# Kernel tuning notes

Hardware: AMD Instinct MI355X
Metric: run time of the kernel (lower is better)

Reference implementation:

```python
import jax, jax.numpy as jnp
import numpy as np

BATCH, IN, HID, OUT = 8192, 1024, 4096, 1000

def _l2norm_rows(w):
    # matches F.normalize(p=2, dim=1) with eps=1e-12
    n = jnp.linalg.norm(w, axis=1, keepdims=True)
    return w / jnp.maximum(n, 1e-12)

def setup_inputs() -> dict:
    key = jax.random.key(0)
    k1, k2, k3 = jax.random.split(key, 3)
    x = jax.random.normal(k1, (BATCH, IN), dtype=jnp.float32)
    kohonen_w = _l2norm_rows(jax.random.normal(k2, (HID, IN), dtype=jnp.float32))
    grossberg_w = _l2norm_rows(jax.random.normal(k3, (OUT, HID), dtype=jnp.float32))
    return {"x": x, "kohonen_w": kohonen_w, "grossberg_w": grossberg_w}

def reference(x, kohonen_w, grossberg_w):
    # x: [B, D]; kohonen_w: [H, D]; grossberg_w: [O, H]
    x2 = jnp.sum(x * x, axis=1, keepdims=True)            # [B, 1]
    w2 = jnp.sum(kohonen_w * kohonen_w, axis=1)           # [H]
    d2 = x2 - 2.0 * (x @ kohonen_w.T) + w2[None, :]       # [B, H]
    winners = jnp.argmin(d2, axis=1)                      # [B] (argmin of dist == argmin of dist^2)
    # one-hot @ grossberg_w.T is exactly a row gather of grossberg_w.T
    output = grossberg_w.T[winners]                       # [B, O]
    return output, winners, x.shape[0]
```

## Files before the change

### kernel.cpp

```cpp
#include <hip/hip_runtime.h>
#include <stdint.h>

#define B_SZ 8192
#define D_SZ 1024
#define H_SZ 4096
#define O_SZ 1000

#define MARGIN 0.0625f

typedef float f32x4 __attribute__((ext_vector_type(4)));
typedef __bf16 bf16x8 __attribute__((ext_vector_type(8)));

static __device__ __forceinline__ uint16_t f2bf(float f) {
  uint32_t u = __float_as_uint(f);
  uint32_t r = (u + 0x7fffu + ((u >> 16) & 1u)) >> 16;
  return (uint16_t)r;
}

__global__ __launch_bounds__(256) void convert_bf16(const float* __restrict__ src,
                                                    ushort4* __restrict__ dst, int n4) {
  int i = blockIdx.x * blockDim.x + threadIdx.x;
  if (i < n4) {
    f32x4 v = reinterpret_cast<const f32x4*>(src)[i];
    ushort4 o;
    o.x = f2bf(v[0]); o.y = f2bf(v[1]); o.z = f2bf(v[2]); o.w = f2bf(v[3]);
    dst[i] = o;
  }
}

__global__ __launch_bounds__(64) void w2_kernel(const float* __restrict__ w,
                                                double* __restrict__ w2d) {
  const int h = blockIdx.x;
  const int l = threadIdx.x;
  const f32x4* wr = reinterpret_cast<const f32x4*>(w + (size_t)h * D_SZ);
  double s = 0.0;
#pragma unroll
  for (int j = 0; j < 4; ++j) {
    f32x4 v = wr[j * 64 + l];
    s += (double)v[0] * v[0] + (double)v[1] * v[1] + (double)v[2] * v[2] + (double)v[3] * v[3];
  }
#pragma unroll
  for (int m = 32; m; m >>= 1) s += __shfl_xor(s, m);
  if (l == 0) w2d[h] = s;
}

#define LPITCH 72
__global__ __launch_bounds__(256) void kohonen_gemm(const uint16_t* __restrict__ xb,
                                                    const uint16_t* __restrict__ wb,
                                                    float* __restrict__ tmax64,
                                                    unsigned long long* __restrict__ tmask64) {
  __shared__ uint16_t As[128 * LPITCH];
  __shared__ uint16_t Bs[128 * LPITCH];
  const int tid = threadIdx.x;
  const int bm = blockIdx.x, bn = blockIdx.y;
  const int lane = tid & 63, wv = tid >> 6;
  const int wm = wv >> 1, wn = wv & 1;
  f32x4 acc[4][4] = {};

  const int sr = tid >> 3;
  const int sp = tid & 7;
  const uint16_t* xrow = xb + (size_t)(bm * 128) * D_SZ;
  const uint16_t* wrow = wb + (size_t)(bn * 128) * D_SZ;

  for (int kt = 0; kt < D_SZ / 64; ++kt) {
    __syncthreads();
#pragma unroll
    for (int i = 0; i < 4; ++i) {
      const int r = sr + i * 32;
      const int4 va = *reinterpret_cast<const int4*>(xrow + (size_t)r * D_SZ + kt * 64 + sp * 8);
      *reinterpret_cast<int4*>(&As[r * LPITCH + sp * 8]) = va;
      const int4 vb = *reinterpret_cast<const int4*>(wrow + (size_t)r * D_SZ + kt * 64 + sp * 8);
      *reinterpret_cast<int4*>(&Bs[r * LPITCH + sp * 8]) = vb;
    }
    __syncthreads();
#pragma unroll
    for (int s = 0; s < 2; ++s) {
      bf16x8 a[4], b[4];
      const int col = s * 32 + (lane >> 4) * 8;
#pragma unroll
      for (int f = 0; f < 4; ++f) {
        a[f] = *reinterpret_cast<const bf16x8*>(&As[(wm * 64 + f * 16 + (lane & 15)) * LPITCH + col]);
        b[f] = *reinterpret_cast<const bf16x8*>(&Bs[(wn * 64 + f * 16 + (lane & 15)) * LPITCH + col]);
      }
#pragma unroll
      for (int fm = 0; fm < 4; ++fm)
#pragma unroll
        for (int fn = 0; fn < 4; ++fn)
          acc[fm][fn] = __builtin_amdgcn_mfma_f32_16x16x32_bf16(a[fm], b[fn], acc[fm][fn], 0, 0, 0);
    }
  }

  const int tile = bn * 2 + wn;
  const int colid = lane & 15;
  const int g = lane >> 4;
#pragma unroll
  for (int fm = 0; fm < 4; ++fm) {
    float v[4];
#pragma unroll
    for (int j = 0; j < 4; ++j)
      v[j] = fmaxf(fmaxf(acc[fm][0][j], acc[fm][1][j]), fmaxf(acc[fm][2][j], acc[fm][3][j]));
#pragma unroll
    for (int m = 1; m < 16; m <<= 1) {
#pragma unroll
      for (int j = 0; j < 4; ++j) v[j] = fmaxf(v[j], __shfl_xor(v[j], m));
    }
    unsigned long long mk[4];
#pragma unroll
    for (int j = 0; j < 4; ++j) {
      unsigned long long b = 0;
      const float thr = v[j] - MARGIN;
#pragma unroll
      for (int fn = 0; fn < 4; ++fn)
        if (acc[fm][fn][j] >= thr) b |= 1ull << (fn * 16 + colid);
      mk[j] = b;
    }
#pragma unroll
    for (int m = 1; m < 16; m <<= 1) {
#pragma unroll
      for (int j = 0; j < 4; ++j) mk[j] |= __shfl_xor(mk[j], m);
    }
    if (colid == 0) {
#pragma unroll
      for (int j = 0; j < 4; ++j) {
        const int row = bm * 128 + wm * 64 + fm * 16 + g * 4 + j;
        tmax64[(size_t)row * 64 + tile] = v[j];
        tmask64[(size_t)row * 64 + tile] = mk[j];
      }
    }
  }
}

__global__ __launch_bounds__(64) void rescore2(const float* __restrict__ x,
                                               const float* __restrict__ w,
                                               const double* __restrict__ w2d,
                                               const float* __restrict__ tmax64,
                                               const unsigned long long* __restrict__ tmask64,
                                               int* __restrict__ winners,
                                               float* __restrict__ winners_f) {
  const int row = blockIdx.x;
  const int l = threadIdx.x;

  f32x4 xr[4];
  const f32x4* xp = reinterpret_cast<const f32x4*>(x + (size_t)row * D_SZ);
#pragma unroll
  for (int j = 0; j < 4; ++j) xr[j] = xp[j * 64 + l];

  const float pmax = tmax64[(size_t)row * 64 + l];
  const unsigned long long pmask = tmask64[(size_t)row * 64 + l];
  float M = pmax;
#pragma unroll
  for (int m = 1; m < 64; m <<= 1) M = fmaxf(M, __shfl_xor(M, m));
  const float thr = M - MARGIN;

  double bestS = -1e300;
  int bestI = 0x7fffffff;

  unsigned long long bits = __ballot(pmax >= thr && pmask != 0ull);
  while (bits) {
    const int src = __ffsll(bits) - 1;
    unsigned long long tmask = __shfl(pmask, src);
    const int tile = src;
    while (tmask) {
      const int b = __ffsll(tmask) - 1;
      const int h = tile * 64 + b;
      const f32x4* wp = reinterpret_cast<const f32x4*>(w + (size_t)h * D_SZ);
      double dot = 0.0;
#pragma unroll
      for (int j = 0; j < 4; ++j) {
        f32x4 wv = wp[j * 64 + l];
        dot += (double)xr[j][0] * wv[0] + (double)xr[j][1] * wv[1] +
               (double)xr[j][2] * wv[2] + (double)xr[j][3] * wv[3];
      }
#pragma unroll
      for (int m = 32; m; m >>= 1) dot += __shfl_xor(dot, m);
      const double sc = 2.0 * dot - w2d[h];
      if (sc > bestS || (sc == bestS && h < bestI)) { bestS = sc; bestI = h; }
      tmask &= tmask - 1;
    }
    bits &= bits - 1;
  }

  if (l == 0) { winners[row] = bestI; winners_f[row] = (float)bestI; }
}

__global__ __launch_bounds__(256) void transpose_g(const float* __restrict__ g,
                                                   float* __restrict__ gt) {
  __shared__ float t[32][33];
  const int h0 = blockIdx.x * 32;
  const int o0 = blockIdx.y * 32;
  const int lx = threadIdx.x & 31, ly = threadIdx.x >> 5;
  for (int i = ly; i < 32; i += 8) {
    const int o = o0 + i;
    t[i][lx] = (o < O_SZ) ? g[(size_t)o * H_SZ + (h0 + lx)] : 0.f;
  }
  __syncthreads();
  for (int i = ly; i < 32; i += 8) {
    const int o = o0 + lx;
    if (o < O_SZ) gt[(size_t)(h0 + i) * O_SZ + o] = t[lx][i];
  }
}

__global__ __launch_bounds__(256) void gather_out(const float* __restrict__ gt,
                                                  const int* __restrict__ winners,
                                                  float* __restrict__ out) {
  const int row = blockIdx.x;
  const int wsel = winners[row];
  const f32x4* src = reinterpret_cast<const f32x4*>(gt + (size_t)wsel * O_SZ);
  f32x4* dst = reinterpret_cast<f32x4*>(out + (size_t)row * O_SZ);
  if (threadIdx.x < O_SZ / 4) dst[threadIdx.x] = src[threadIdx.x];
  if (row == 0 && threadIdx.x == 0)
    out[(size_t)B_SZ * O_SZ + B_SZ] = (float)B_SZ;
}

extern "C" void kernel_launch(void* const* d_in, const int* in_sizes, int n_in,
                              void* d_out, int out_size, void* d_ws, size_t ws_size,
                              hipStream_t stream) {
  const float* x  = (const float*)d_in[0];
  const float* kw = (const float*)d_in[1];
  const float* gw = (const float*)d_in[2];
  float* out = (float*)d_out;
  char* ws = (char*)d_ws;

  uint16_t*           xb   = (uint16_t*)(ws);
  uint16_t*           wb   = (uint16_t*)(ws + 16777216);
  float*              tmx  = (float*)   (ws + 25165824);
  unsigned long long* tmk  = (unsigned long long*)(ws + 27262976);
  int*                wins = (int*)     (ws + 31457280);
  double*             w2d  = (double*)  (ws + 31490048);
  float*              gt   = (float*)   (ws);

  convert_bf16<<<(B_SZ * D_SZ / 4 + 255) / 256, 256, 0, stream>>>(x, (ushort4*)xb, B_SZ * D_SZ / 4);
  convert_bf16<<<(H_SZ * D_SZ / 4 + 255) / 256, 256, 0, stream>>>(kw, (ushort4*)wb, H_SZ * D_SZ / 4);
  w2_kernel<<<H_SZ, 64, 0, stream>>>(kw, w2d);

  dim3 g1(B_SZ / 128, H_SZ / 128);
  kohonen_gemm<<<g1, 256, 0, stream>>>(xb, wb, tmx, tmk);

  rescore2<<<B_SZ, 64, 0, stream>>>(x, kw, w2d, tmx, tmk, wins, out + (size_t)B_SZ * O_SZ);

  dim3 g3(H_SZ / 32, (O_SZ + 31) / 32);
  transpose_g<<<g3, 256, 0, stream>>>(gw, gt);

  gather_out<<<B_SZ, 256, 0, stream>>>(gt, wins, out);
}
```

Measured before the change: 139.1 us.

## Load GEMM tiles directly into LDS with global_load_lds and XOR swizzle

Replaces the register-staged global-to-LDS copy in the Kohonen GEMM with direct global_load_lds DMA transfers of 16 bytes per lane. The padded LDS layout becomes an unpadded 128-byte-pitch layout, with an XOR swizzle applied on both the load mapping and the fragment reads to limit bank conflicts. This is meant to cut VGPR traffic and the instructions spent staging tiles, at the cost of an explicit vmcnt wait and a more fragile address mapping.

```diff
diff --git a/kernel.cpp b/kernel.cpp
--- a/kernel.cpp
+++ b/kernel.cpp
@@ -44,43 +44,60 @@
   if (l == 0) w2d[h] = s;
 }
 
-#define LPITCH 72
 __global__ __launch_bounds__(256) void kohonen_gemm(const uint16_t* __restrict__ xb,
                                                     const uint16_t* __restrict__ wb,
                                                     float* __restrict__ tmax64,
                                                     unsigned long long* __restrict__ tmask64) {
-  __shared__ uint16_t As[128 * LPITCH];
-  __shared__ uint16_t Bs[128 * LPITCH];
+  __shared__ uint16_t As[8192];
+  __shared__ uint16_t Bs[8192];
   const int tid = threadIdx.x;
   const int bm = blockIdx.x, bn = blockIdx.y;
   const int lane = tid & 63, wv = tid >> 6;
   const int wm = wv >> 1, wn = wv & 1;
   f32x4 acc[4][4] = {};
 
-  const int sr = tid >> 3;
-  const int sp = tid & 7;
   const uint16_t* xrow = xb + (size_t)(bm * 128) * D_SZ;
   const uint16_t* wrow = wb + (size_t)(bn * 128) * D_SZ;
 
+  int srow[4], spart[4];
+#pragma unroll
+  for (int i = 0; i < 4; ++i) {
+    const int c_lin = (wv * 4 + i) * 64 + lane;
+    const int c_src = c_lin ^ ((((c_lin >> 5) & 1)) << 1);
+    srow[i] = c_src >> 3;
+    spart[i] = c_src & 7;
+  }
+
+  const int r15 = lane & 15, g = lane >> 4;
+  const int xorv = (r15 & 4) ? 32 : 0;
+
   for (int kt = 0; kt < D_SZ / 64; ++kt) {
     __syncthreads();
 #pragma unroll
     for (int i = 0; i < 4; ++i) {
-      const int r = sr + i * 32;
-      const int4 va = *reinterpret_cast<const int4*>(xrow + (size_t)r * D_SZ + kt * 64 + sp * 8);
-      *reinterpret_cast<int4*>(&As[r * LPITCH + sp * 8]) = va;
-      const int4 vb = *reinterpret_cast<const int4*>(wrow + (size_t)r * D_SZ + kt * 64 + sp * 8);
-      *reinterpret_cast<int4*>(&Bs[r * LPITCH + sp * 8]) = vb;
-    }
+      const uint16_t* ga = xrow + (size_t)srow[i] * D_SZ + kt * 64 + spart[i] * 8;
+      __builtin_amdgcn_global_load_lds(
+          (const __attribute__((address_space(1))) uint32_t*)ga,
+          (__attribute__((address_space(3))) uint32_t*)((char*)As + ((wv * 4 + i) << 10)),
+          16, 0, 0);
+      const uint16_t* gb = wrow + (size_t)srow[i] * D_SZ + kt * 64 + spart[i] * 8;
+      __builtin_amdgcn_global_load_lds(
+          (const __attribute__((address_space(1))) uint32_t*)gb,
+          (__attribute__((address_space(3))) uint32_t*)((char*)Bs + ((wv * 4 + i) << 10)),
+          16, 0, 0);
+    }
+    asm volatile("s_waitcnt vmcnt(0)" ::: "memory");
     __syncthreads();
 #pragma unroll
     for (int s = 0; s < 2; ++s) {
       bf16x8 a[4], b[4];
-      const int col = s * 32 + (lane >> 4) * 8;
+      const int cb = s * 64 + g * 16;
 #pragma unroll
       for (int f = 0; f < 4; ++f) {
-        a[f] = *reinterpret_cast<const bf16x8*>(&As[(wm * 64 + f * 16 + (lane & 15)) * LPITCH + col]);
-        b[f] = *reinterpret_cast<const bf16x8*>(&Bs[(wn * 64 + f * 16 + (lane & 15)) * LPITCH + col]);
+        const int ra = (wm * 64 + f * 16 + r15) * 128 + cb;
+        a[f] = *reinterpret_cast<const bf16x8*>((const char*)As + (ra ^ xorv));
+        const int rb = (wn * 64 + f * 16 + r15) * 128 + cb;
+        b[f] = *reinterpret_cast<const bf16x8*>((const char*)Bs + (rb ^ xorv));
       }
 #pragma unroll
       for (int fm = 0; fm < 4; ++fm)
@@ -92,7 +109,6 @@
 
   const int tile = bn * 2 + wn;
   const int colid = lane & 15;
-  const int g = lane >> 4;
 #pragma unroll
   for (int fm = 0; fm < 4; ++fm) {
     float v[4];
@@ -107,12 +123,12 @@
     unsigned long long mk[4];
 #pragma unroll
     for (int j = 0; j < 4; ++j) {
-      unsigned long long b = 0;
+      unsigned long long bmask = 0;
       const float thr = v[j] - MARGIN;
 #pragma unroll
       for (int fn = 0; fn < 4; ++fn)
-        if (acc[fm][fn][j] >= thr) b |= 1ull << (fn * 16 + colid);
-      mk[j] = b;
+        if (acc[fm][fn][j] >= thr) bmask |= 1ull << (fn * 16 + colid);
+      mk[j] = bmask;
     }
 #pragma unroll
     for (int m = 1; m < 16; m <<= 1) {
```

After: 146.2 us. 5.1% more time.

## Rework Kohonen GEMM with async LDS double buffering and 32x32 MFMA

Applied to the files above, without the earlier changes.

Rewrites the bf16 GEMM main loop to stage tiles straight from global memory into LDS with global_load_lds, double-buffered so the next K tile loads while the current one computes. Uses XOR-swizzled LDS addressing instead of padding, and switches to 32x32x16 MFMA with four accumulators per wave. Also remaps block IDs to group tiles for cache locality and sets launch bounds for two blocks per CU. The epilogue is rewritten for the new accumulator layout. This adds hand-written waitcnt and barrier logic that must stay correct.

```diff
diff --git a/kernel.cpp b/kernel.cpp
--- a/kernel.cpp
+++ b/kernel.cpp
@@ -9,6 +9,7 @@
 #define MARGIN 0.0625f
 
 typedef float f32x4 __attribute__((ext_vector_type(4)));
+typedef float f32x16 __attribute__((ext_vector_type(16)));
 typedef __bf16 bf16x8 __attribute__((ext_vector_type(8)));
 
 static __device__ __forceinline__ uint16_t f2bf(float f) {
@@ -44,87 +45,98 @@
   if (l == 0) w2d[h] = s;
 }
 
-#define LPITCH 72
-__global__ __launch_bounds__(256) void kohonen_gemm(const uint16_t* __restrict__ xb,
-                                                    const uint16_t* __restrict__ wb,
-                                                    float* __restrict__ tmax64,
-                                                    unsigned long long* __restrict__ tmask64) {
-  __shared__ uint16_t As[128 * LPITCH];
-  __shared__ uint16_t Bs[128 * LPITCH];
+__global__ __launch_bounds__(256, 2) void kohonen_gemm(const uint16_t* __restrict__ xb,
+                                                       const uint16_t* __restrict__ wb,
+                                                       float* __restrict__ tmax64,
+                                                       unsigned long long* __restrict__ tmask64) {
+  __shared__ __align__(16) char As[32768];
+  __shared__ __align__(16) char Bs[32768];
   const int tid = threadIdx.x;
-  const int bm = blockIdx.x, bn = blockIdx.y;
   const int lane = tid & 63, wv = tid >> 6;
   const int wm = wv >> 1, wn = wv & 1;
-  f32x4 acc[4][4] = {};
-
-  const int sr = tid >> 3;
-  const int sp = tid & 7;
+  const int l31 = lane & 31, hi = lane >> 5;
+
+  const int bid = blockIdx.x;
+  const int wg = (bid & 7) * 256 + (bid >> 3);
+  const int bm = wg >> 5, bn = wg & 31;
+
   const uint16_t* xrow = xb + (size_t)(bm * 128) * D_SZ;
   const uint16_t* wrow = wb + (size_t)(bn * 128) * D_SZ;
 
-  for (int kt = 0; kt < D_SZ / 64; ++kt) {
-    __syncthreads();
+  f32x16 acc00 = {}, acc01 = {}, acc10 = {}, acc11 = {};
+
+  const int st_row = (lane >> 3);
+  const int st_part = (lane & 7) ^ (((lane >> 3) & 3) << 1);
+  auto stage = [&](int sp, int kt) {
 #pragma unroll
     for (int i = 0; i < 4; ++i) {
-      const int r = sr + i * 32;
-      const int4 va = *reinterpret_cast<const int4*>(xrow + (size_t)r * D_SZ + kt * 64 + sp * 8);
-      *reinterpret_cast<int4*>(&As[r * LPITCH + sp * 8]) = va;
-      const int4 vb = *reinterpret_cast<const int4*>(wrow + (size_t)r * D_SZ + kt * 64 + sp * 8);
-      *reinterpret_cast<int4*>(&Bs[r * LPITCH + sp * 8]) = vb;
-    }
-    __syncthreads();
-#pragma unroll
-    for (int s = 0; s < 2; ++s) {
-      bf16x8 a[4], b[4];
-      const int col = s * 32 + (lane >> 4) * 8;
-#pragma unroll
-      for (int f = 0; f < 4; ++f) {
-        a[f] = *reinterpret_cast<const bf16x8*>(&As[(wm * 64 + f * 16 + (lane & 15)) * LPITCH + col]);
-        b[f] = *reinterpret_cast<const bf16x8*>(&Bs[(wn * 64 + f * 16 + (lane & 15)) * LPITCH + col]);
-      }
-#pragma unroll
-      for (int fm = 0; fm < 4; ++fm)
-#pragma unroll
-        for (int fn = 0; fn < 4; ++fn)
-          acc[fm][fn] = __builtin_amdgcn_mfma_f32_16x16x32_bf16(a[fm], b[fn], acc[fm][fn], 0, 0, 0);
-    }
+      const int blk = wv * 4 + i;
+      const int row = blk * 8 + st_row;
+      const uint16_t* sa = xrow + (size_t)row * D_SZ + kt * 64 + st_part * 8;
+      __builtin_amdgcn_global_load_lds(
+          (const __attribute__((address_space(1))) uint32_t*)sa,
+          (__attribute__((address_space(3))) uint32_t*)(As + sp * 16384 + blk * 1024),
+          16, 0, 0);
+      const uint16_t* sb = wrow + (size_t)row * D_SZ + kt * 64 + st_part * 8;
+      __builtin_amdgcn_global_load_lds(
+          (const __attribute__((address_space(1))) uint32_t*)sb,
+          (__attribute__((address_space(3))) uint32_t*)(Bs + sp * 16384 + blk * 1024),
+          16, 0, 0);
+    }
+  };
+
+  auto ldfrag = [&](const char* base, int row, int ks) -> bf16x8 {
+    const int byte = (row * 128 + ks * 32 + hi * 16) ^ ((row & 3) << 5);
+    return *reinterpret_cast<const bf16x8*>(base + byte);
+  };
+
+  stage(0, 0);
+
+  for (int t = 0; t < 16; ++t) {
+    const int rp = t & 1, sp = rp ^ 1;
+    if (t < 15) {
+      stage(sp, t + 1);
+      asm volatile("s_waitcnt vmcnt(8)" ::: "memory");
+    } else {
+      asm volatile("s_waitcnt vmcnt(0)" ::: "memory");
+    }
+    __builtin_amdgcn_s_barrier();
+    const char* Ab = As + rp * 16384;
+    const char* Bb = Bs + rp * 16384;
+#pragma unroll
+    for (int ks = 0; ks < 4; ++ks) {
+      bf16x8 a0 = ldfrag(Ab, wm * 64 + l31, ks);
+      bf16x8 a1 = ldfrag(Ab, wm * 64 + 32 + l31, ks);
+      bf16x8 b0 = ldfrag(Bb, wn * 64 + l31, ks);
+      bf16x8 b1 = ldfrag(Bb, wn * 64 + 32 + l31, ks);
+      acc00 = __builtin_amdgcn_mfma_f32_32x32x16_bf16(a0, b0, acc00, 0, 0, 0);
+      acc01 = __builtin_amdgcn_mfma_f32_32x32x16_bf16(a0, b1, acc01, 0, 0, 0);
+      acc10 = __builtin_amdgcn_mfma_f32_32x32x16_bf16(a1, b0, acc10, 0, 0, 0);
+      acc11 = __builtin_amdgcn_mfma_f32_32x32x16_bf16(a1, b1, acc11, 0, 0, 0);
+    }
+    asm volatile("s_waitcnt lgkmcnt(0)" ::: "memory");
+    __builtin_amdgcn_s_barrier();
   }
 
   const int tile = bn * 2 + wn;
-  const int colid = lane & 15;
-  const int g = lane >> 4;
-#pragma unroll
-  for (int fm = 0; fm < 4; ++fm) {
-    float v[4];
-#pragma unroll
-    for (int j = 0; j < 4; ++j)
-      v[j] = fmaxf(fmaxf(acc[fm][0][j], acc[fm][1][j]), fmaxf(acc[fm][2][j], acc[fm][3][j]));
-#pragma unroll
-    for (int m = 1; m < 16; m <<= 1) {
-#pragma unroll
-      for (int j = 0; j < 4; ++j) v[j] = fmaxf(v[j], __shfl_xor(v[j], m));
-    }
-    unsigned long long mk[4];
-#pragma unroll
-    for (int j = 0; j < 4; ++j) {
-      unsigned long long b = 0;
-      const float thr = v[j] - MARGIN;
-#pragma unroll
-      for (int fn = 0; fn < 4; ++fn)
-        if (acc[fm][fn][j] >= thr) b |= 1ull << (fn * 16 + colid);
-      mk[j] = b;
-    }
-#pragma unroll
-    for (int m = 1; m < 16; m <<= 1) {
-#pragma unroll
-      for (int j = 0; j < 4; ++j) mk[j] |= __shfl_xor(mk[j], m);
-    }
-    if (colid == 0) {
-#pragma unroll
-      for (int j = 0; j < 4; ++j) {
-        const int row = bm * 128 + wm * 64 + fm * 16 + g * 4 + j;
-        tmax64[(size_t)row * 64 + tile] = v[j];
-        tmask64[(size_t)row * 64 + tile] = mk[j];
+#pragma unroll
+  for (int mi = 0; mi < 2; ++mi) {
+    const f32x16 c0 = mi ? acc10 : acc00;
+    const f32x16 c1 = mi ? acc11 : acc01;
+#pragma unroll
+    for (int r = 0; r < 16; ++r) {
+      float v = fmaxf(c0[r], c1[r]);
+#pragma unroll
+      for (int s = 1; s < 32; s <<= 1) v = fmaxf(v, __shfl_xor(v, s));
+      const float thr = v - MARGIN;
+      unsigned long long mk = (c0[r] >= thr ? (1ull << l31) : 0ull) |
+                              (c1[r] >= thr ? (1ull << (32 + l31)) : 0ull);
+#pragma unroll
+      for (int s = 1; s < 32; s <<= 1) mk |= __shfl_xor(mk, s);
+      if (l31 == 0) {
+        const int row = bm * 128 + wm * 64 + mi * 32 + (r & 3) + 8 * (r >> 2) + 4 * hi;
+        tmax64[(size_t)row * 64 + tile] = v;
+        tmask64[(size_t)row * 64 + tile] = mk;
       }
     }
   }
@@ -233,8 +245,7 @@
   convert_bf16<<<(H_SZ * D_SZ / 4 + 255) / 256, 256, 0, stream>>>(kw, (ushort4*)wb, H_SZ * D_SZ / 4);
   w2_kernel<<<H_SZ, 64, 0, stream>>>(kw, w2d);
 
-  dim3 g1(B_SZ / 128, H_SZ / 128);
-  kohonen_gemm<<<g1, 256, 0, stream>>>(xb, wb, tmx, tmk);
+  kohonen_gemm<<<2048, 256, 0, stream>>>(xb, wb, tmx, tmk);
 
   rescore2<<<B_SZ, 64, 0, stream>>>(x, kw, w2d, tmx, tmk, wins, out + (size_t)B_SZ * O_SZ);
 
```

Result: slower. 193.3 us (+39.0%).
